# Kernel optimization log

Hardware: AMD Instinct MI355X
Metric: run time of the kernel (lower is better)

## Reference

```python
import jax, jax.numpy as jnp
import numpy as np

N = 100000
E = 1600000
D_IN = 64
D_HID = 64
D_OUT = 64


def setup_inputs() -> dict:
    key = jax.random.key(0)
    ks = jax.random.split(key, 12)
    x = jax.random.normal(ks[0], (N, D_IN), dtype=jnp.float32)
    edge_index = jax.random.randint(ks[1], (2, E), 0, N, dtype=jnp.int64)
    s1 = 1.0 / np.sqrt(D_IN)
    s2 = 1.0 / np.sqrt(D_HID)
    return {
        "x": x,
        "edge_index": edge_index,
        "W1l": jax.random.uniform(ks[2], (D_HID, D_IN), jnp.float32, -s1, s1),
        "b1l": jax.random.uniform(ks[3], (D_HID,), jnp.float32, -s1, s1),
        "W1r": jax.random.uniform(ks[4], (D_HID, D_IN), jnp.float32, -s1, s1),
        "W2l": jax.random.uniform(ks[5], (D_HID, D_HID), jnp.float32, -s2, s2),
        "b2l": jax.random.uniform(ks[6], (D_HID,), jnp.float32, -s2, s2),
        "W2r": jax.random.uniform(ks[7], (D_HID, D_HID), jnp.float32, -s2, s2),
        "Wout": jax.random.uniform(ks[8], (D_OUT, D_HID), jnp.float32, -s2, s2),
        "bout": jax.random.uniform(ks[9], (D_OUT,), jnp.float32, -s2, s2),
        "drop": 0,
    }


def _sage_conv(x, src, dst, Wl, bl, Wr, n_nodes):
    # PyG SAGEConv, aggr='mean': out = lin_l(mean_j x_j) + lin_r(x_i)
    msg = x[src]                                            # [E, d] gather
    agg = jax.ops.segment_sum(msg, dst, num_segments=n_nodes)
    deg = jax.ops.segment_sum(jnp.ones((src.shape[0],), x.dtype), dst,
                              num_segments=n_nodes)
    mean = agg / jnp.maximum(deg, 1.0)[:, None]             # empty neighborhoods -> 0
    return mean @ Wl.T + bl + x @ Wr.T


def reference(x, edge_index, W1l, b1l, W1r, W2l, b2l, W2r, Wout, bout, drop):
    src, dst = edge_index[0], edge_index[1]
    n = x.shape[0]
    # dropout is identity in eval mode (training=False); drop unused
    h = jax.nn.relu(_sage_conv(x, src, dst, W1l, b1l, W1r, n))
    h = jax.nn.relu(_sage_conv(h, src, dst, W2l, b2l, W2r, n))
    logits = h @ Wout.T + bout
    return jax.nn.log_softmax(logits, axis=1)
```

## Files before the change

kernel.cpp:

```cpp
#include <hip/hip_runtime.h>


#define TB 256
#define TBA 1024
#define CAPB 2560

typedef __attribute__((ext_vector_type(8))) short bf16x8;
typedef __attribute__((ext_vector_type(4))) float f32x4;
typedef __attribute__((ext_vector_type(2))) float f32x2;

__device__ __forceinline__ short bf16c(float f) {
  union { float f; unsigned u; } v; v.f = f;
  unsigned r = (v.u + 0x7FFFu + ((v.u >> 16) & 1u)) >> 16;
  return (short)r;
}

__device__ __forceinline__ bf16x8 ld_bf8(const float* p) {
  float4 a = *(const float4*)p;
  float4 b = *(const float4*)(p + 4);
  bf16x8 r;
  r[0] = bf16c(a.x); r[1] = bf16c(a.y); r[2] = bf16c(a.z); r[3] = bf16c(a.w);
  r[4] = bf16c(b.x); r[5] = bf16c(b.y); r[6] = bf16c(b.z); r[7] = bf16c(b.w);
  return r;
}

__global__ __launch_bounds__(1024) void k_binA(
    const int* __restrict__ ei, int E,
    int* __restrict__ bucket_fill, unsigned int* __restrict__ bucketData, int NB) {
  __shared__ int hist[1024];
  __shared__ int base[1024];
  __shared__ int s_nz;
  if (threadIdx.x == 0) s_nz = 0;
  for (int i = threadIdx.x; i < NB; i += TBA) hist[i] = 0;
  __syncthreads();
  int nz = 0;
  for (int i = threadIdx.x; i < 2048; i += TBA) nz |= ei[2 * i + 1];
  if (nz) atomicOr(&s_nz, 1);
  __syncthreads();
  bool m64 = (s_nz == 0);

  long long e0 = (long long)E * blockIdx.x / gridDim.x;
  long long e1 = (long long)E * (blockIdx.x + 1) / gridDim.x;
  for (long long e = e0 + threadIdx.x; e < e1; e += TBA) {
    int dst = m64 ? ((const int2*)ei)[(long long)E + e].x : ei[(long long)E + e];
    atomicAdd(&hist[dst >> 7], 1);
  }
  __syncthreads();
  for (int b = threadIdx.x; b < NB; b += TBA) {
    int c = hist[b];
    base[b] = c ? atomicAdd(&bucket_fill[b], c) : 0;
    hist[b] = 0;
  }
  __syncthreads();
  for (long long e = e0 + threadIdx.x; e < e1; e += TBA) {
    int src, dst;
    if (m64) {
      src = ((const int2*)ei)[e].x;
      dst = ((const int2*)ei)[(long long)E + e].x;
    } else {
      src = ei[e];
      dst = ei[(long long)E + e];
    }
    int b = dst >> 7;
    int pos = base[b] + atomicAdd(&hist[b], 1);
    if (pos < CAPB)
      bucketData[(size_t)b * CAPB + pos] =
          ((unsigned)(dst & 127) << 24) | (unsigned)src;
  }
}

__global__ __launch_bounds__(256) void k_binB(
    const unsigned int* __restrict__ bucketData, const int* __restrict__ bucket_fill,
    int* __restrict__ colp, int* __restrict__ cnt) {
  __shared__ unsigned int slice[128 * 64];
  __shared__ int lcnt[128];
  int b = blockIdx.x;
  for (int i = threadIdx.x; i < 128; i += TB) lcnt[i] = 0;
  __syncthreads();
  int fcnt = bucket_fill[b];
  if (fcnt > CAPB) fcnt = CAPB;
  const unsigned int* bd = bucketData + (size_t)b * CAPB;
  for (int k = threadIdx.x; k < fcnt; k += TB) {
    unsigned int rec = bd[k];
    int dl = rec >> 24;
    int pos = atomicAdd(&lcnt[dl], 1);
    if (pos < 64) slice[(dl << 6) + pos] = rec & 0xFFFFFFu;
  }
  __syncthreads();
  size_t obase = (size_t)b * (128 * 64);
  for (int i = threadIdx.x * 4; i < 128 * 64; i += TB * 4) {
    *(uint4*)(colp + obase + i) = *(const uint4*)(slice + i);
  }
  int node0 = b << 7;
  for (int i = threadIdx.x; i < 128; i += TB) cnt[node0 + i] = lcnt[i];
}

__global__ __launch_bounds__(256) void k_xform_mfma(
    const float* xin, const float* __restrict__ Wl, const float* __restrict__ Wr,
    const float* __restrict__ bl, unsigned short* __restrict__ y, float* zout, int n) {
  int lane = threadIdx.x & 63;
  int quad = lane >> 4, m = lane & 15;
  int w0 = (blockIdx.x * blockDim.x + threadIdx.x) >> 6;
  int nw = (gridDim.x * blockDim.x) >> 6;

  bf16x8 bfrag[8][2];
  float bias[4];
#pragma unroll
  for (int t = 0; t < 8; ++t) {
    const float* W = (t < 4) ? Wl : Wr;
    int row = (t & 3) * 16 + m;
#pragma unroll
    for (int s = 0; s < 2; ++s)
      bfrag[t][s] = ld_bf8(W + row * 64 + s * 32 + quad * 8);
  }
#pragma unroll
  for (int t = 0; t < 4; ++t) bias[t] = bl[t * 16 + m];

  int nT = (n + 15) >> 4;
  for (int tile = w0; tile < nT; tile += nw) {
    int node0 = tile << 4;
    int mrow = node0 + m;
    if (mrow >= n) mrow = n - 1;
    const float* xr = xin + (size_t)mrow * 64;
    bf16x8 a0 = ld_bf8(xr + quad * 8);
    bf16x8 a1 = ld_bf8(xr + 32 + quad * 8);

    f32x4 acc[8];
#pragma unroll
    for (int t = 0; t < 8; ++t) {
      f32x4 z4 = {0.f, 0.f, 0.f, 0.f};
      z4 = __builtin_amdgcn_mfma_f32_16x16x32_bf16(a0, bfrag[t][0], z4, 0, 0, 0);
      acc[t] = __builtin_amdgcn_mfma_f32_16x16x32_bf16(a1, bfrag[t][1], z4, 0, 0, 0);
    }

#pragma unroll
    for (int r = 0; r < 4; ++r) {
      int node = node0 + quad * 4 + r;
      if (node >= n) break;
      size_t rb = (size_t)node * 64 + m;
#pragma unroll
      for (int t = 0; t < 4; ++t)
        y[rb + t * 16] = (unsigned short)bf16c(acc[t][r]);
#pragma unroll
      for (int t = 0; t < 4; ++t)
        zout[rb + t * 16] = acc[t + 4][r] + bias[t];
    }
  }
}

__global__ __launch_bounds__(256) void k_aggr(
    const unsigned short* __restrict__ yb, const int* __restrict__ cnt,
    const int* __restrict__ colp, float* zio, int n) {
  const unsigned int* y = (const unsigned int*)yb;
  int lane = threadIdx.x & 63;
  int wv = (blockIdx.x * blockDim.x + threadIdx.x) >> 6;
  int g16 = lane & 48;
  int lig = lane & 15;
  int sub = lig >> 3;
  int fo = (lig & 7) * 4;

  int node = (wv << 2) + (g16 >> 4);
  bool act = node < n;
  int cn = act ? node : 0;
  int deg = cnt[cn];
  int jcap = deg < 64 ? deg : 64;
  size_t crow = (size_t)cn << 6;
  int cidxA = colp[crow + lig];
  int cidxB = colp[crow + 16 + lig];

  int wmax = jcap;
  wmax = max(wmax, __shfl_xor(wmax, 16, 64));
  wmax = max(wmax, __shfl_xor(wmax, 32, 64));

  f32x2 acc[4];
#pragma unroll
  for (int k = 0; k < 4; ++k) acc[k] = (f32x2){0.f, 0.f};

#define ACCUM(U)                                                              \
  do {                                                                        \
    acc[0] += (f32x2){__uint_as_float((U).x << 16),                           \
                      __uint_as_float((U).x & 0xFFFF0000u)};                  \
    acc[1] += (f32x2){__uint_as_float((U).y << 16),                           \
                      __uint_as_float((U).y & 0xFFFF0000u)};                  \
    acc[2] += (f32x2){__uint_as_float((U).z << 16),                          \
                      __uint_as_float((U).z & 0xFFFF0000u)};                  \
    acc[3] += (f32x2){__uint_as_float((U).w << 16),                           \
                      __uint_as_float((U).w & 0xFFFF0000u)};                  \
  } while (0)

  {
    int lim = wmax < 16 ? wmax : 16;
    for (int s = 0; s < lim; s += 2) {
      int slot = s + sub;
      int c = __shfl(cidxA, g16 | slot, 64);
      if (slot < jcap) {
        uint4 v = *(const uint4*)(y + ((size_t)c << 5) + fo);
        ACCUM(v);
      }
    }
  }
  if (wmax > 16) {
    int lim = (wmax < 32 ? wmax : 32) - 16;
    for (int s = 0; s < lim; s += 2) {
      int slot = s + sub;
      int c = __shfl(cidxB, g16 | slot, 64);
      if (slot + 16 < jcap) {
        uint4 v = *(const uint4*)(y + ((size_t)c << 5) + fo);
        ACCUM(v);
      }
    }
  }
  if (wmax > 32) {
    int cidxC = colp[crow + 32 + lig];
    int cidxD = colp[crow + 48 + lig];
    {
      int lim = (wmax < 48 ? wmax : 48) - 32;
      for (int s = 0; s < lim; s += 2) {
        int slot = s + sub;
        int c = __shfl(cidxC, g16 | slot, 64);
        if (slot + 32 < jcap) {
          uint4 v = *(const uint4*)(y + ((size_t)c << 5) + fo);
          ACCUM(v);
        }
      }
    }
    if (wmax > 48) {
      int lim = wmax - 48;
      for (int s = 0; s < lim; s += 2) {
        int slot = s + sub;
        int c = __shfl(cidxD, g16 | slot, 64);
        if (slot + 48 < jcap) {
          uint4 v = *(const uint4*)(y + ((size_t)c << 5) + fo);
          ACCUM(v);
        }
      }
    }
  }
#undef ACCUM

#pragma unroll
  for (int k = 0; k < 4; ++k) {
    acc[k].x += __shfl_xor(acc[k].x, 8, 64);
    acc[k].y += __shfl_xor(acc[k].y, 8, 64);
  }

  if (act && sub == 0) {
    float inv = (deg > 0) ? 1.0f / (float)deg : 0.f;
    float* zp = zio + ((size_t)node << 6) + fo * 2;
    float4 z0 = *(float4*)zp;
    float4 z1 = *(float4*)(zp + 4);
    z0.x = fmaxf(fmaf(acc[0].x, inv, z0.x), 0.f);
    z0.y = fmaxf(fmaf(acc[0].y, inv, z0.y), 0.f);
    z0.z = fmaxf(fmaf(acc[1].x, inv, z0.z), 0.f);
    z0.w = fmaxf(fmaf(acc[1].y, inv, z0.w), 0.f);
    z1.x = fmaxf(fmaf(acc[2].x, inv, z1.x), 0.f);
    z1.y = fmaxf(fmaf(acc[2].y, inv, z1.y), 0.f);
    z1.z = fmaxf(fmaf(acc[3].x, inv, z1.z), 0.f);
    z1.w = fmaxf(fmaf(acc[3].y, inv, z1.w), 0.f);
    *(float4*)zp = z0;
    *(float4*)(zp + 4) = z1;
  }
}

__global__ __launch_bounds__(256) void k_out_mfma(
    const float* __restrict__ h, const float* __restrict__ Wo,
    const float* __restrict__ bo, float* __restrict__ out, int n) {
  int lane = threadIdx.x & 63;
  int quad = lane >> 4, m = lane & 15;
  int w0 = (blockIdx.x * blockDim.x + threadIdx.x) >> 6;
  int nw = (gridDim.x * blockDim.x) >> 6;

  bf16x8 bfrag[4][2];
  float bias[4];
#pragma unroll
  for (int t = 0; t < 4; ++t) {
    int row = t * 16 + m;
#pragma unroll
    for (int s = 0; s < 2; ++s)
      bfrag[t][s] = ld_bf8(Wo + row * 64 + s * 32 + quad * 8);
    bias[t] = bo[t * 16 + m];
  }

  int nT = (n + 15) >> 4;
  for (int tile = w0; tile < nT; tile += nw) {
    int node0 = tile << 4;
    int mrow = node0 + m;
    if (mrow >= n) mrow = n - 1;
    const float* xr = h + (size_t)mrow * 64;
    bf16x8 a0 = ld_bf8(xr + quad * 8);
    bf16x8 a1 = ld_bf8(xr + 32 + quad * 8);

    f32x4 acc[4];
#pragma unroll
    for (int t = 0; t < 4; ++t) {
      f32x4 z4 = {0.f, 0.f, 0.f, 0.f};
      z4 = __builtin_amdgcn_mfma_f32_16x16x32_bf16(a0, bfrag[t][0], z4, 0, 0, 0);
      acc[t] = __builtin_amdgcn_mfma_f32_16x16x32_bf16(a1, bfrag[t][1], z4, 0, 0, 0);
    }

#pragma unroll
    for (int r = 0; r < 4; ++r) {
      int node = node0 + quad * 4 + r;
      if (node >= n) break;
      float l0 = acc[0][r] + bias[0];
      float l1 = acc[1][r] + bias[1];
      float l2 = acc[2][r] + bias[2];
      float l3 = acc[3][r] + bias[3];
      float mx = fmaxf(fmaxf(l0, l1), fmaxf(l2, l3));
#pragma unroll
      for (int off = 1; off <= 8; off <<= 1) mx = fmaxf(mx, __shfl_xor(mx, off, 64));
      float s = expf(l0 - mx) + expf(l1 - mx) + expf(l2 - mx) + expf(l3 - mx);
#pragma unroll
      for (int off = 1; off <= 8; off <<= 1) s += __shfl_xor(s, off, 64);
      float ls = logf(s);
      size_t rb = (size_t)node * 64 + m;
      out[rb + 0]  = l0 - mx - ls;
      out[rb + 16] = l1 - mx - ls;
      out[rb + 32] = l2 - mx - ls;
      out[rb + 48] = l3 - mx - ls;
    }
  }
}

extern "C" void kernel_launch(void* const* d_in, const int* in_sizes, int n_in,
                              void* d_out, int out_size, void* d_ws, size_t ws_size,
                              hipStream_t stream) {
  const float* x    = (const float*)d_in[0];
  const int*   ei   = (const int*)d_in[1];
  const float* W1l  = (const float*)d_in[2];
  const float* b1l  = (const float*)d_in[3];
  const float* W1r  = (const float*)d_in[4];
  const float* W2l  = (const float*)d_in[5];
  const float* b2l  = (const float*)d_in[6];
  const float* W2r  = (const float*)d_in[7];
  const float* Wout = (const float*)d_in[8];
  const float* bout = (const float*)d_in[9];
  int N = in_sizes[0] / 64;
  int E = in_sizes[1] / 2;
  int NB = (N + 127) >> 7;

  char* p = (char*)d_ws;
  auto carve = [&](size_t bytes) {
    char* r = p;
    p += (bytes + 255) & ~(size_t)255;
    return r;
  };
  int* bucket_fill   = (int*)carve((size_t)NB * 4);
  int* cnt           = (int*)carve((size_t)NB * 128 * 4);
  int* colp          = (int*)carve((size_t)NB * 128 * 64 * 4);
  unsigned short* y  = (unsigned short*)carve((size_t)N * 64 * 2);
  float* z           = (float*)carve((size_t)N * 64 * 4);
  unsigned int* bucketData = (unsigned int*)z;

  hipMemsetAsync(bucket_fill, 0, (size_t)NB * 4, stream);

  k_binA<<<256, TBA, 0, stream>>>(ei, E, bucket_fill, bucketData, NB);
  k_binB<<<NB, TB, 0, stream>>>(bucketData, bucket_fill, colp, cnt);

  int aggr_blocks = (N + 15) / 16;
  k_xform_mfma<<<512, TB, 0, stream>>>(x, W1l, W1r, b1l, y, z, N);
  k_aggr<<<aggr_blocks, TB, 0, stream>>>(y, cnt, colp, z, N);
  k_xform_mfma<<<512, TB, 0, stream>>>(z, W2l, W2r, b2l, y, z, N);
  k_aggr<<<aggr_blocks, TB, 0, stream>>>(y, cnt, colp, z, N);
  k_out_mfma<<<512, TB, 0, stream>>>(z, Wout, bout, (float*)d_out, N);
}
```

Baseline: 250.6 us.

## Fuse neighbor aggregation with following MFMA transform and log-softmax output

Merges each mean-aggregation pass with the next dense stage: the aggregated and ReLU'd hidden tile for 16 nodes is built per wave in shared memory, then fed straight into the bf16 MFMA transform (layer 2) or the output projection with log-softmax. This removes the fp32 hidden-state write and re-read between kernels and two kernel launches. It uses separate y buffers for the two layers and updates z in place per wave. Each wave now aggregates 16 nodes serially instead of 4, which may lower memory-level parallelism per wave.

Result: slower. 324.4 us (+29.5%).

```diff
diff --git a/kernel.cpp b/kernel.cpp
--- a/kernel.cpp
+++ b/kernel.cpp
@@ -15,13 +15,15 @@
   return (short)r;
 }
 
-__device__ __forceinline__ bf16x8 ld_bf8(const float* p) {
-  float4 a = *(const float4*)p;
-  float4 b = *(const float4*)(p + 4);
+__device__ __forceinline__ bf16x8 cvt_bf8(float4 a, float4 b) {
   bf16x8 r;
   r[0] = bf16c(a.x); r[1] = bf16c(a.y); r[2] = bf16c(a.z); r[3] = bf16c(a.w);
   r[4] = bf16c(b.x); r[5] = bf16c(b.y); r[6] = bf16c(b.z); r[7] = bf16c(b.w);
   return r;
+}
+
+__device__ __forceinline__ bf16x8 ld_bf8(const float* p) {
+  return cvt_bf8(*(const float4*)p, *(const float4*)(p + 4));
 }
 
 __global__ __launch_bounds__(1024) void k_binA(
@@ -95,84 +97,22 @@
   for (int i = threadIdx.x; i < 128; i += TB) cnt[node0 + i] = lcnt[i];
 }
 
-__global__ __launch_bounds__(256) void k_xform_mfma(
-    const float* xin, const float* __restrict__ Wl, const float* __restrict__ Wr,
-    const float* __restrict__ bl, unsigned short* __restrict__ y, float* zout, int n) {
-  int lane = threadIdx.x & 63;
-  int quad = lane >> 4, m = lane & 15;
-  int w0 = (blockIdx.x * blockDim.x + threadIdx.x) >> 6;
-  int nw = (gridDim.x * blockDim.x) >> 6;
-
-  bf16x8 bfrag[8][2];
-  float bias[4];
-#pragma unroll
-  for (int t = 0; t < 8; ++t) {
-    const float* W = (t < 4) ? Wl : Wr;
-    int row = (t & 3) * 16 + m;
-#pragma unroll
-    for (int s = 0; s < 2; ++s)
-      bfrag[t][s] = ld_bf8(W + row * 64 + s * 32 + quad * 8);
-  }
-#pragma unroll
-  for (int t = 0; t < 4; ++t) bias[t] = bl[t * 16 + m];
-
-  int nT = (n + 15) >> 4;
-  for (int tile = w0; tile < nT; tile += nw) {
-    int node0 = tile << 4;
-    int mrow = node0 + m;
-    if (mrow >= n) mrow = n - 1;
-    const float* xr = xin + (size_t)mrow * 64;
-    bf16x8 a0 = ld_bf8(xr + quad * 8);
-    bf16x8 a1 = ld_bf8(xr + 32 + quad * 8);
-
-    f32x4 acc[8];
-#pragma unroll
-    for (int t = 0; t < 8; ++t) {
-      f32x4 z4 = {0.f, 0.f, 0.f, 0.f};
-      z4 = __builtin_amdgcn_mfma_f32_16x16x32_bf16(a0, bfrag[t][0], z4, 0, 0, 0);
-      acc[t] = __builtin_amdgcn_mfma_f32_16x16x32_bf16(a1, bfrag[t][1], z4, 0, 0, 0);
-    }
-
-#pragma unroll
-    for (int r = 0; r < 4; ++r) {
-      int node = node0 + quad * 4 + r;
-      if (node >= n) break;
-      size_t rb = (size_t)node * 64 + m;
-#pragma unroll
-      for (int t = 0; t < 4; ++t)
-        y[rb + t * 16] = (unsigned short)bf16c(acc[t][r]);
-#pragma unroll
-      for (int t = 0; t < 4; ++t)
-        zout[rb + t * 16] = acc[t + 4][r] + bias[t];
-    }
-  }
-}
-
-__global__ __launch_bounds__(256) void k_aggr(
-    const unsigned short* __restrict__ yb, const int* __restrict__ cnt,
-    const int* __restrict__ colp, float* zio, int n) {
-  const unsigned int* y = (const unsigned int*)yb;
-  int lane = threadIdx.x & 63;
-  int wv = (blockIdx.x * blockDim.x + threadIdx.x) >> 6;
-  int g16 = lane & 48;
-  int lig = lane & 15;
-  int sub = lig >> 3;
+__device__ __forceinline__ void aggr_node(
+    const unsigned int* __restrict__ y, const int* __restrict__ cnt,
+    const int* __restrict__ colp, int node, int n, int lane,
+    f32x2 acc[4], int& deg) {
+  int g16 = lane & 48, lig = lane & 15, sub = lig >> 3;
   int fo = (lig & 7) * 4;
-
-  int node = (wv << 2) + (g16 >> 4);
   bool act = node < n;
   int cn = act ? node : 0;
-  int deg = cnt[cn];
+  deg = cnt[cn];
   int jcap = deg < 64 ? deg : 64;
   size_t crow = (size_t)cn << 6;
   int cidxA = colp[crow + lig];
   int cidxB = colp[crow + 16 + lig];
-
   int wmax = jcap;
   wmax = max(wmax, __shfl_xor(wmax, 16, 64));
   wmax = max(wmax, __shfl_xor(wmax, 32, 64));
-
-  f32x2 acc[4];
 #pragma unroll
   for (int k = 0; k < 4; ++k) acc[k] = (f32x2){0.f, 0.f};
 
@@ -182,7 +122,7 @@
                       __uint_as_float((U).x & 0xFFFF0000u)};                  \
     acc[1] += (f32x2){__uint_as_float((U).y << 16),                           \
                       __uint_as_float((U).y & 0xFFFF0000u)};                  \
-    acc[2] += (f32x2){__uint_as_float((U).z << 16),                          \
+    acc[2] += (f32x2){__uint_as_float((U).z << 16),                           \
                       __uint_as_float((U).z & 0xFFFF0000u)};                  \
     acc[3] += (f32x2){__uint_as_float((U).w << 16),                           \
                       __uint_as_float((U).w & 0xFFFF0000u)};                  \
@@ -243,56 +183,197 @@
     acc[k].x += __shfl_xor(acc[k].x, 8, 64);
     acc[k].y += __shfl_xor(acc[k].y, 8, 64);
   }
-
-  if (act && sub == 0) {
-    float inv = (deg > 0) ? 1.0f / (float)deg : 0.f;
-    float* zp = zio + ((size_t)node << 6) + fo * 2;
-    float4 z0 = *(float4*)zp;
-    float4 z1 = *(float4*)(zp + 4);
-    z0.x = fmaxf(fmaf(acc[0].x, inv, z0.x), 0.f);
-    z0.y = fmaxf(fmaf(acc[0].y, inv, z0.y), 0.f);
-    z0.z = fmaxf(fmaf(acc[1].x, inv, z0.z), 0.f);
-    z0.w = fmaxf(fmaf(acc[1].y, inv, z0.w), 0.f);
-    z1.x = fmaxf(fmaf(acc[2].x, inv, z1.x), 0.f);
-    z1.y = fmaxf(fmaf(acc[2].y, inv, z1.y), 0.f);
-    z1.z = fmaxf(fmaf(acc[3].x, inv, z1.z), 0.f);
-    z1.w = fmaxf(fmaf(acc[3].y, inv, z1.w), 0.f);
-    *(float4*)zp = z0;
-    *(float4*)(zp + 4) = z1;
-  }
-}
-
-__global__ __launch_bounds__(256) void k_out_mfma(
-    const float* __restrict__ h, const float* __restrict__ Wo,
-    const float* __restrict__ bo, float* __restrict__ out, int n) {
+}
+
+__device__ __forceinline__ void build_htile(
+    const unsigned int* __restrict__ y, const int* __restrict__ cnt,
+    const int* __restrict__ colp, const float* __restrict__ zIn,
+    float* __restrict__ ht , int base, int n, int lane) {
+  int g16 = lane & 48, lig = lane & 15;
+#pragma unroll
+  for (int r = 0; r < 4; ++r) {
+    int node = base + r * 4 + (g16 >> 4);
+    f32x2 acc[4];
+    int deg;
+    aggr_node(y, cnt, colp, node, n, lane, acc, deg);
+    if (lig < 8) {
+      float4 h0 = {0.f, 0.f, 0.f, 0.f}, h1 = {0.f, 0.f, 0.f, 0.f};
+      if (node < n) {
+        float inv = (deg > 0) ? 1.0f / (float)deg : 0.f;
+        const float* zp = zIn + ((size_t)node << 6) + lig * 8;
+        float4 z0 = *(const float4*)zp;
+        float4 z1 = *(const float4*)(zp + 4);
+        h0.x = fmaxf(fmaf(acc[0].x, inv, z0.x), 0.f);
+        h0.y = fmaxf(fmaf(acc[0].y, inv, z0.y), 0.f);
+        h0.z = fmaxf(fmaf(acc[1].x, inv, z0.z), 0.f);
+        h0.w = fmaxf(fmaf(acc[1].y, inv, z0.w), 0.f);
+        h1.x = fmaxf(fmaf(acc[2].x, inv, z1.x), 0.f);
+        h1.y = fmaxf(fmaf(acc[2].y, inv, z1.y), 0.f);
+        h1.z = fmaxf(fmaf(acc[3].x, inv, z1.z), 0.f);
+        h1.w = fmaxf(fmaf(acc[3].y, inv, z1.w), 0.f);
+      }
+      int row = r * 4 + (g16 >> 4);
+      *(float4*)(ht + row * 68 + lig * 8) = h0;
+      *(float4*)(ht + row * 68 + lig * 8 + 4) = h1;
+    }
+  }
+}
+
+__global__ __launch_bounds__(256) void k_aggr_xf(
+    const unsigned short* __restrict__ yIn, const int* __restrict__ cnt,
+    const int* __restrict__ colp, const float* zIn,
+    const float* __restrict__ Wl, const float* __restrict__ Wr,
+    const float* __restrict__ bl,
+    unsigned short* __restrict__ yOut, float* zOut, int n) {
+  __shared__ float ht[4][16 * 68];
+  const unsigned int* y = (const unsigned int*)yIn;
+  int tid = threadIdx.x;
+  int w = tid >> 6;
+  int lane = tid & 63;
+  int base = ((blockIdx.x * blockDim.x + tid) >> 6) << 4;
+
+  build_htile(y, cnt, colp, zIn, ht[w], base, n, lane);
+  __syncthreads();
+
+  int quad = lane >> 4, m = lane & 15;
+  bf16x8 bfrag[8][2];
+  float bias[4];
+#pragma unroll
+  for (int t = 0; t < 8; ++t) {
+    const float* W = (t < 4) ? Wl : Wr;
+    int row = (t & 3) * 16 + m;
+#pragma unroll
+    for (int s = 0; s < 2; ++s)
+      bfrag[t][s] = ld_bf8(W + row * 64 + s * 32 + quad * 8);
+  }
+#pragma unroll
+  for (int t = 0; t < 4; ++t) bias[t] = bl[t * 16 + m];
+
+  const float* hrow = ht[w] + m * 68;
+  bf16x8 a0 = cvt_bf8(*(const float4*)(hrow + quad * 8),
+                      *(const float4*)(hrow + quad * 8 + 4));
+  bf16x8 a1 = cvt_bf8(*(const float4*)(hrow + 32 + quad * 8),
+                      *(const float4*)(hrow + 32 + quad * 8 + 4));
+
+  f32x4 acc[8];
+#pragma unroll
+  for (int t = 0; t < 8; ++t) {
+    f32x4 z4 = {0.f, 0.f, 0.f, 0.f};
+    z4 = __builtin_amdgcn_mfma_f32_16x16x32_bf16(a0, bfrag[t][0], z4, 0, 0, 0);
+    acc[t] = __builtin_amdgcn_mfma_f32_16x16x32_bf16(a1, bfrag[t][1], z4, 0, 0, 0);
+  }
+
+#pragma unroll
+  for (int r = 0; r < 4; ++r) {
+    int node = base + quad * 4 + r;
+    if (node >= n) break;
+    size_t rb = (size_t)node * 64 + m;
+#pragma unroll
+    for (int t = 0; t < 4; ++t)
+      yOut[rb + t * 16] = (unsigned short)bf16c(acc[t][r]);
+#pragma unroll
+    for (int t = 0; t < 4; ++t)
+      zOut[rb + t * 16] = acc[t + 4][r] + bias[t];
+  }
+}
+
+__global__ __launch_bounds__(256) void k_aggr_out(
+    const unsigned short* __restrict__ yIn, const int* __restrict__ cnt,
+    const int* __restrict__ colp, const float* __restrict__ zIn,
+    const float* __restrict__ Wo, const float* __restrict__ bo,
+    float* __restrict__ out, int n) {
+  __shared__ float ht[4][16 * 68];
+  const unsigned int* y = (const unsigned int*)yIn;
+  int tid = threadIdx.x;
+  int w = tid >> 6;
+  int lane = tid & 63;
+  int base = ((blockIdx.x * blockDim.x + tid) >> 6) << 4;
+
+  build_htile(y, cnt, colp, zIn, ht[w], base, n, lane);
+  __syncthreads();
+
+  int quad = lane >> 4, m = lane & 15;
+  bf16x8 bfrag[4][2];
+  float bias[4];
+#pragma unroll
+  for (int t = 0; t < 4; ++t) {
+    int row = t * 16 + m;
+#pragma unroll
+    for (int s = 0; s < 2; ++s)
+      bfrag[t][s] = ld_bf8(Wo + row * 64 + s * 32 + quad * 8);
+    bias[t] = bo[t * 16 + m];
+  }
+
+  const float* hrow = ht[w] + m * 68;
+  bf16x8 a0 = cvt_bf8(*(const float4*)(hrow + quad * 8),
+                      *(const float4*)(hrow + quad * 8 + 4));
+  bf16x8 a1 = cvt_bf8(*(const float4*)(hrow + 32 + quad * 8),
+                      *(const float4*)(hrow + 32 + quad * 8 + 4));
+
+  f32x4 acc[4];
+#pragma unroll
+  for (int t = 0; t < 4; ++t) {
+    f32x4 z4 = {0.f, 0.f, 0.f, 0.f};
+    z4 = __builtin_amdgcn_mfma_f32_16x16x32_bf16(a0, bfrag[t][0], z4, 0, 0, 0);
+    acc[t] = __builtin_amdgcn_mfma_f32_16x16x32_bf16(a1, bfrag[t][1], z4, 0, 0, 0);
+  }
+
+#pragma unroll
+  for (int r = 0; r < 4; ++r) {
+    int node = base + quad * 4 + r;
+    if (node >= n) break;
+    float l0 = acc[0][r] + bias[0];
+    float l1 = acc[1][r] + bias[1];
+    float l2 = acc[2][r] + bias[2];
+    float l3 = acc[3][r] + bias[3];
+    float mx = fmaxf(fmaxf(l0, l1), fmaxf(l2, l3));
+#pragma unroll
+    for (int off = 1; off <= 8; off <<= 1) mx = fmaxf(mx, __shfl_xor(mx, off, 64));
+    float s = expf(l0 - mx) + expf(l1 - mx) + expf(l2 - mx) + expf(l3 - mx);
+#pragma unroll
+    for (int off = 1; off <= 8; off <<= 1) s += __shfl_xor(s, off, 64);
+    float ls = logf(s);
+    size_t rb = (size_t)node * 64 + m;
+    out[rb + 0]  = l0 - mx - ls;
+    out[rb + 16] = l1 - mx - ls;
+    out[rb + 32] = l2 - mx - ls;
+    out[rb + 48] = l3 - mx - ls;
+  }
+}
+
+__global__ __launch_bounds__(256) void k_xform_mfma(
+    const float* xin, const float* __restrict__ Wl, const float* __restrict__ Wr,
+    const float* __restrict__ bl, unsigned short* __restrict__ y, float* zout, int n) {
   int lane = threadIdx.x & 63;
   int quad = lane >> 4, m = lane & 15;
   int w0 = (blockIdx.x * blockDim.x + threadIdx.x) >> 6;
   int nw = (gridDim.x * blockDim.x) >> 6;
 
-  bf16x8 bfrag[4][2];
+  bf16x8 bfrag[8][2];
   float bias[4];
 #pragma unroll
-  for (int t = 0; t < 4; ++t) {
-    int row = t * 16 + m;
+  for (int t = 0; t < 8; ++t) {
+    const float* W = (t < 4) ? Wl : Wr;
+    int row = (t & 3) * 16 + m;
 #pragma unroll
     for (int s = 0; s < 2; ++s)
-      bfrag[t][s] = ld_bf8(Wo + row * 64 + s * 32 + quad * 8);
-    bias[t] = bo[t * 16 + m];
-  }
+      bfrag[t][s] = ld_bf8(W + row * 64 + s * 32 + quad * 8);
+  }
+#pragma unroll
+  for (int t = 0; t < 4; ++t) bias[t] = bl[t * 16 + m];
 
   int nT = (n + 15) >> 4;
   for (int tile = w0; tile < nT; tile += nw) {
     int node0 = tile << 4;
     int mrow = node0 + m;
     if (mrow >= n) mrow = n - 1;
-    const float* xr = h + (size_t)mrow * 64;
+    const float* xr = xin + (size_t)mrow * 64;
     bf16x8 a0 = ld_bf8(xr + quad * 8);
     bf16x8 a1 = ld_bf8(xr + 32 + quad * 8);
 
-    f32x4 acc[4];
-#pragma unroll
-    for (int t = 0; t < 4; ++t) {
+    f32x4 acc[8];
+#pragma unroll
+    for (int t = 0; t < 8; ++t) {
       f32x4 z4 = {0.f, 0.f, 0.f, 0.f};
       z4 = __builtin_amdgcn_mfma_f32_16x16x32_bf16(a0, bfrag[t][0], z4, 0, 0, 0);
       acc[t] = __builtin_amdgcn_mfma_f32_16x16x32_bf16(a1, bfrag[t][1], z4, 0, 0, 0);
@@ -302,22 +383,13 @@
     for (int r = 0; r < 4; ++r) {
       int node = node0 + quad * 4 + r;
       if (node >= n) break;
-      float l0 = acc[0][r] + bias[0];
-      float l1 = acc[1][r] + bias[1];
-      float l2 = acc[2][r] + bias[2];
-      float l3 = acc[3][r] + bias[3];
-      float mx = fmaxf(fmaxf(l0, l1), fmaxf(l2, l3));
-#pragma unroll
-      for (int off = 1; off <= 8; off <<= 1) mx = fmaxf(mx, __shfl_xor(mx, off, 64));
-      float s = expf(l0 - mx) + expf(l1 - mx) + expf(l2 - mx) + expf(l3 - mx);
-#pragma unroll
-      for (int off = 1; off <= 8; off <<= 1) s += __shfl_xor(s, off, 64);
-      float ls = logf(s);
       size_t rb = (size_t)node * 64 + m;
-      out[rb + 0]  = l0 - mx - ls;
-      out[rb + 16] = l1 - mx - ls;
-      out[rb + 32] = l2 - mx - ls;
-      out[rb + 48] = l3 - mx - ls;
+#pragma unroll
+      for (int t = 0; t < 4; ++t)
+        y[rb + t * 16] = (unsigned short)bf16c(acc[t][r]);
+#pragma unroll
+      for (int t = 0; t < 4; ++t)
+        zout[rb + t * 16] = acc[t + 4][r] + bias[t];
     }
   }
 }
@@ -348,7 +420,8 @@
   int* bucket_fill   = (int*)carve((size_t)NB * 4);
   int* cnt           = (int*)carve((size_t)NB * 128 * 4);
   int* colp          = (int*)carve((size_t)NB * 128 * 64 * 4);
-  unsigned short* y  = (unsigned short*)carve((size_t)N * 64 * 2);
+  unsigned short* y1 = (unsigned short*)carve((size_t)N * 64 * 2);
+  unsigned short* y2 = (unsigned short*)carve((size_t)N * 64 * 2);
   float* z           = (float*)carve((size_t)N * 64 * 4);
   unsigned int* bucketData = (unsigned int*)z;
 
@@ -357,10 +430,10 @@
   k_binA<<<256, TBA, 0, stream>>>(ei, E, bucket_fill, bucketData, NB);
   k_binB<<<NB, TB, 0, stream>>>(bucketData, bucket_fill, colp, cnt);
 
-  int aggr_blocks = (N + 15) / 16;
-  k_xform_mfma<<<512, TB, 0, stream>>>(x, W1l, W1r, b1l, y, z, N);
-  k_aggr<<<aggr_blocks, TB, 0, stream>>>(y, cnt, colp, z, N);
-  k_xform_mfma<<<512, TB, 0, stream>>>(z, W2l, W2r, b2l, y, z, N);
-  k_aggr<<<aggr_blocks, TB, 0, stream>>>(y, cnt, colp, z, N);
-  k_out_mfma<<<512, TB, 0, stream>>>(z, Wout, bout, (float*)d_out, N);
-}
+  int fuse_blocks = (N + 63) / 64;
+  k_xform_mfma<<<512, TB, 0, stream>>>(x, W1l, W1r, b1l, y1, z, N);
+  k_aggr_xf<<<fuse_blocks, TB, 0, stream>>>(y1, cnt, colp, z, W2l, W2r, b2l,
+                                            y2, z, N);
+  k_aggr_out<<<fuse_blocks, TB, 0, stream>>>(y2, cnt, colp, z, Wout, bout,
+                                             (float*)d_out, N);
+}
```
